# Kernel tuning notes

Measured on AMD Instinct MI355X. Metric: run time of the kernel, lower is better.

The kernel has to match this reference:

```python
import jax, jax.numpy as jnp
import numpy as np

N = 65536          # nodes
E = 1_048_576      # edges (avg degree 16)
IN_DIM = 16        # input_irreps = 16x0e
OUT_DIM = 8        # output_irreps = 8x0e
S_MUL = 32         # hidden 0e multiplicity
V_MUL = 16         # hidden 1o multiplicity
HID = S_MUL + 3 * V_MUL  # 80
LAYERS = 3
DEG = 16.0


def fctp(feat, eattr, w1, w2, w3, w4):
    """FullyConnectedTensorProduct(hidden x '1x0e+1x1o' -> hidden) per edge.
    Paths: 0e*0e->0e, 1o*1o->0e (dot, CG 1/sqrt(3)), 0e*1o->1o, 1o*0e->1o.
    Path weights mix multiplicities; e3nn-style fan-in normalization."""
    s1 = feat[:, :S_MUL]                         # [E, 32]
    v1 = feat[:, S_MUL:].reshape(-1, V_MUL, 3)   # [E, 16, 3]
    s2 = eattr[:, 0]                             # [E]
    v2 = eattr[:, 1:4]                           # [E, 3]
    c = 1.0 / np.sqrt(2.0)  # two paths per output irrep
    out_s = c * (jnp.einsum('ea,e,ac->ec', s1, s2, w1) / np.sqrt(S_MUL)
                 + jnp.einsum('eak,ek,ac->ec', v1, v2, w2) / np.sqrt(3.0 * V_MUL))
    out_v = c * (jnp.einsum('ea,ek,ac->eck', s1, v2, w3) / np.sqrt(S_MUL)
                 + jnp.einsum('eak,e,ac->eck', v1, s2, w4) / np.sqrt(V_MUL))
    return jnp.concatenate([out_s, out_v.reshape(-1, 3 * V_MUL)], axis=-1)


def setup_inputs() -> dict:
    key = jax.random.key(0)
    ks = jax.random.split(key, 12)
    inp = {
        'x': jax.random.normal(ks[0], (N, IN_DIM), jnp.float32),
        'edge_index': jax.random.randint(ks[1], (2, E), 0, N, jnp.int64 if jax.config.jax_enable_x64 else jnp.int32),
        'edge_attr': jax.random.normal(ks[2], (E, 4), jnp.float32),
        'W_in': jax.random.normal(ks[3], (IN_DIM, HID), jnp.float32) / np.sqrt(IN_DIM),
        'b_in': jnp.zeros((HID,), jnp.float32),
        'tp_w1': jax.random.normal(ks[4], (LAYERS, S_MUL, S_MUL), jnp.float32),
        'tp_w2': jax.random.normal(ks[5], (LAYERS, V_MUL, S_MUL), jnp.float32),
        'tp_w3': jax.random.normal(ks[6], (LAYERS, S_MUL, V_MUL), jnp.float32),
        'tp_w4': jax.random.normal(ks[7], (LAYERS, V_MUL, V_MUL), jnp.float32),
        'W_out': jax.random.normal(ks[8], (HID, OUT_DIM), jnp.float32) / np.sqrt(HID),
        'b_out': jnp.zeros((OUT_DIM,), jnp.float32),
    }
    return inp


def reference(x, edge_index, edge_attr, W_in, b_in, tp_w1, tp_w2, tp_w3, tp_w4, W_out, b_out):
    src, dst = edge_index[0], edge_index[1]
    h = x @ W_in + b_in                                   # [N, 80]
    for l in range(LAYERS):
        m = fctp(h[src], edge_attr, tp_w1[l], tp_w2[l], tp_w3[l], tp_w4[l])  # [E, 80]
        h = jax.ops.segment_sum(m, dst, num_segments=N) / np.sqrt(DEG)       # [N, 80]
    h = jax.nn.relu(h)
    return h @ W_out + b_out                              # [N, 8]
```

## Files before the change

kernel.cpp:

```cpp
#include <hip/hip_runtime.h>

#define NN 65536
#define NE 1048576
#define HID 80

typedef unsigned int u32;
typedef unsigned short u16;
typedef unsigned long long u64;

__device__ __forceinline__ u16 f2bf(float f) {
  u32 u = __float_as_uint(f);
  u = (u + 0x7fffu + ((u >> 16) & 1u)) >> 16;
  return (u16)u;
}
__device__ __forceinline__ float bfhi(u32 packed) {
  return __uint_as_float(packed & 0xffff0000u);
}
__device__ __forceinline__ float bflo(u32 packed) {
  return __uint_as_float(packed << 16);
}

__global__ __launch_bounds__(256) void k_in(const float* __restrict__ x,
    const float* __restrict__ W, const float* __restrict__ b,
    u16* __restrict__ hmain, u16* __restrict__ htail) {
  int idx = blockIdx.x * 256 + threadIdx.x;
  if (idx >= NN * HID) return;
  int n = idx / HID, l = idx % HID;
  const float* xr = x + n * 16;
  float acc = b[l];
#pragma unroll
  for (int k = 0; k < 16; k++) acc += xr[k] * W[k * HID + l];
  u16 v = f2bf(acc);
  if (l < 64) hmain[(size_t)n * 64 + l] = v;
  else htail[(size_t)n * 16 + (l - 64)] = v;
}

__global__ __launch_bounds__(256) void k_hist(const int* __restrict__ dst,
    int* __restrict__ counts, int* __restrict__ rank, int* __restrict__ dcnt) {
  if (blockIdx.x == 0 && threadIdx.x < 16) dcnt[threadIdx.x] = 0;
  int base = blockIdx.x * 2048 + threadIdx.x;
#pragma unroll
  for (int k = 0; k < 8; k++) {
    int idx = base + k * 256;
    rank[idx] = atomicAdd(&counts[dst[idx]], 1);
  }
}

__global__ __launch_bounds__(256) void k_nb_scan(const int* __restrict__ counts,
    int* __restrict__ offsets, int* __restrict__ blocksum,
    int* __restrict__ dcnt, int* __restrict__ brank, int* __restrict__ bidx) {
  __shared__ int sc[256];
  int t = threadIdx.x;
  if (blockIdx.x < 64) {
    int base = blockIdx.x * 1024 + t * 4;
    int p0 = (counts[base] + 7) & ~7;
    int p1 = (counts[base + 1] + 7) & ~7;
    int p2 = (counts[base + 2] + 7) & ~7;
    int p3 = (counts[base + 3] + 7) & ~7;
    int s = p0 + p1 + p2 + p3;
    sc[t] = s;
    __syncthreads();
    for (int d = 1; d < 256; d <<= 1) {
      int v = (t >= d) ? sc[t - d] : 0;
      __syncthreads();
      sc[t] += v;
      __syncthreads();
    }
    int excl = sc[t] - s;
    offsets[base] = excl;
    offsets[base + 1] = excl + p0;
    offsets[base + 2] = excl + p0 + p1;
    offsets[base + 3] = excl + p0 + p1 + p2;
    if (t == 255) blocksum[blockIdx.x] = sc[255];
  } else {
    int n = (blockIdx.x - 64) * 256 + t;
    int degp = (counts[n] + 7) & ~7;
    int b = 15 - min(degp >> 3, 15);
    int lane = t & 63;
    int base = 0;
#pragma unroll 1
    for (int bb = 0; bb < 16; bb++) {
      u64 m = __ballot(b == bb);
      if (b == bb) {
        int leader = __ffsll((long long)m) - 1;
        int lr = __popcll(m & ((lane == 63) ? ~0ull >> 1 : ((1ull << lane) - 1)));
        int bs = 0;
        if (lane == leader) bs = atomicAdd(&dcnt[bb], __popcll(m));
        bs = __shfl(bs, leader, 64);
        base = bs + lr;
      }
    }
    brank[n] = base;
    bidx[n] = b;
  }
}

__global__ __launch_bounds__(64) void k_scan2(int* __restrict__ blocksum,
                                              int* __restrict__ dcnt) {
  int t = threadIdx.x;
  if (blockIdx.x == 0) {
    int v = blocksum[t];
    int incl = v;
#pragma unroll
    for (int d = 1; d < 64; d <<= 1) {
      int o = __shfl_up(incl, d, 64);
      if (t >= d) incl += o;
    }
    blocksum[t] = incl - v;
  } else {
    if (t >= 16) return;
    int v = dcnt[t];
    int incl = v;
#pragma unroll
    for (int d = 1; d < 16; d <<= 1) {
      int o = __shfl_up(incl, d, 64);
      if (t >= d) incl += o;
    }
    dcnt[t] = incl - v;
  }
}

__global__ __launch_bounds__(256) void k_node_fin(int* __restrict__ offsets,
    const int* __restrict__ blocksum, const int* __restrict__ counts,
    u16* __restrict__ esrc, uint2* __restrict__ eat,
    const int* __restrict__ dcnt, const int* __restrict__ brank,
    const int* __restrict__ bidx, int* __restrict__ nperm) {
  int n = blockIdx.x * 256 + threadIdx.x;
  int off = offsets[n] + blocksum[n >> 10];
  offsets[n] = off;
  int deg = counts[n];
  int degp = (deg + 7) & ~7;
  uint2 z2 = make_uint2(0u, 0u);
  for (int e = deg; e < degp; e++) {
    esrc[off + e] = 0;
    eat[off + e] = z2;
  }
  nperm[dcnt[bidx[n]] + brank[n]] = n;
}

__global__ __launch_bounds__(256) void k_fill(const int* __restrict__ src,
    const int* __restrict__ dst, const float4* __restrict__ eattr,
    const int* __restrict__ offsets, const int* __restrict__ rank,
    u16* __restrict__ esrc, uint2* __restrict__ eat) {
  int base = blockIdx.x * 2048 + threadIdx.x;
#pragma unroll
  for (int k = 0; k < 8; k++) {
    int idx = base + k * 256;
    int d = dst[idx];
    float4 ea = eattr[idx];
    int s = src[idx];
    u32 c01 = (u32)f2bf(ea.x) | ((u32)f2bf(ea.y) << 16);
    u32 c23 = (u32)f2bf(ea.z) | ((u32)f2bf(ea.w) << 16);
    int pos = offsets[d] + rank[idx];
    esrc[pos] = (u16)s;
    eat[pos] = make_uint2(c01, c23);
  }
}

template <int LAST>
__global__ __launch_bounds__(128, 3) void k_msg(const u16* __restrict__ hmain,
    const u16* __restrict__ htail, u16* __restrict__ omain,
    u16* __restrict__ otail,
    const float* __restrict__ w1, const float* __restrict__ w2,
    const float* __restrict__ w3, const float* __restrict__ w4,
    const int* __restrict__ offsets, const int* __restrict__ counts,
    const int* __restrict__ nperm, const u16* __restrict__ esrc,
    const uint2* __restrict__ eat, const float* __restrict__ Wout,
    const float* __restrict__ bout, float* __restrict__ outp) {
  __shared__ float Rlds[8][4][81];
  int tid = threadIdx.x;
  const int q = tid >> 4;
  const int c = tid & 15;
  const int n = nperm[blockIdx.x * 8 + q];

  float R[4][5];
#pragma unroll
  for (int j = 0; j < 4; j++)
#pragma unroll
    for (int i = 0; i < 5; i++) R[j][i] = 0.f;

  const int start = offsets[n];
  const int degp = (counts[n] + 7) & ~7;
  const int B = degp >> 3;
  const uint2* hrow = (const uint2*)hmain + c;
  const u16* trow = htail + c;

  int i = 0;
  for (; i + 2 <= B; i += 2) {
    const int baseA = start + 8 * i;
    const int baseB = baseA + 8;
    u32 sA[8], sB[8];
    uint2 aA[8], aB[8];
#pragma unroll
    for (int k = 0; k < 8; k++) sA[k] = esrc[baseA + k];
#pragma unroll
    for (int k = 0; k < 8; k++) aA[k] = eat[baseA + k];
#pragma unroll
    for (int k = 0; k < 8; k++) sB[k] = esrc[baseB + k];
#pragma unroll
    for (int k = 0; k < 8; k++) aB[k] = eat[baseB + k];
    uint2 hA[8], hB[8];
    u32 tA[8], tB[8];
#pragma unroll
    for (int k = 0; k < 8; k++) {
      size_t s16 = (size_t)sA[k] * 16;
      hA[k] = hrow[s16];
      tA[k] = trow[s16];
    }
#pragma unroll
    for (int k = 0; k < 8; k++) {
      size_t s16 = (size_t)sB[k] * 16;
      hB[k] = hrow[s16];
      tB[k] = trow[s16];
    }
#pragma unroll
    for (int k = 0; k < 8; k++) {
      float A0 = bflo(hA[k].x), A1 = bfhi(hA[k].x);
      float A2 = bflo(hA[k].y), A3 = bfhi(hA[k].y);
      float A4 = bflo(tA[k]);
      float f0 = bflo(aA[k].x), f1 = bfhi(aA[k].x);
      float f2 = bflo(aA[k].y), f3 = bfhi(aA[k].y);
      R[0][0] += f0 * A0; R[0][1] += f0 * A1; R[0][2] += f0 * A2;
      R[0][3] += f0 * A3; R[0][4] += f0 * A4;
      R[1][0] += f1 * A0; R[1][1] += f1 * A1; R[1][2] += f1 * A2;
      R[1][3] += f1 * A3; R[1][4] += f1 * A4;
      R[2][0] += f2 * A0; R[2][1] += f2 * A1; R[2][2] += f2 * A2;
      R[2][3] += f2 * A3; R[2][4] += f2 * A4;
      R[3][0] += f3 * A0; R[3][1] += f3 * A1; R[3][2] += f3 * A2;
      R[3][3] += f3 * A3; R[3][4] += f3 * A4;
    }
#pragma unroll
    for (int k = 0; k < 8; k++) {
      float A0 = bflo(hB[k].x), A1 = bfhi(hB[k].x);
      float A2 = bflo(hB[k].y), A3 = bfhi(hB[k].y);
      float A4 = bflo(tB[k]);
      float f0 = bflo(aB[k].x), f1 = bfhi(aB[k].x);
      float f2 = bflo(aB[k].y), f3 = bfhi(aB[k].y);
      R[0][0] += f0 * A0; R[0][1] += f0 * A1; R[0][2] += f0 * A2;
      R[0][3] += f0 * A3; R[0][4] += f0 * A4;
      R[1][0] += f1 * A0; R[1][1] += f1 * A1; R[1][2] += f1 * A2;
      R[1][3] += f1 * A3; R[1][4] += f1 * A4;
      R[2][0] += f2 * A0; R[2][1] += f2 * A1; R[2][2] += f2 * A2;
      R[2][3] += f2 * A3; R[2][4] += f2 * A4;
      R[3][0] += f3 * A0; R[3][1] += f3 * A1; R[3][2] += f3 * A2;
      R[3][3] += f3 * A3; R[3][4] += f3 * A4;
    }
  }
  if (i < B) {
    const int baseA = start + 8 * i;
    u32 sA[8];
    uint2 aA[8];
#pragma unroll
    for (int k = 0; k < 8; k++) sA[k] = esrc[baseA + k];
#pragma unroll
    for (int k = 0; k < 8; k++) aA[k] = eat[baseA + k];
    uint2 hA[8];
    u32 tA[8];
#pragma unroll
    for (int k = 0; k < 8; k++) {
      size_t s16 = (size_t)sA[k] * 16;
      hA[k] = hrow[s16];
      tA[k] = trow[s16];
    }
#pragma unroll
    for (int k = 0; k < 8; k++) {
      float A0 = bflo(hA[k].x), A1 = bfhi(hA[k].x);
      float A2 = bflo(hA[k].y), A3 = bfhi(hA[k].y);
      float A4 = bflo(tA[k]);
      float f0 = bflo(aA[k].x), f1 = bfhi(aA[k].x);
      float f2 = bflo(aA[k].y), f3 = bfhi(aA[k].y);
      R[0][0] += f0 * A0; R[0][1] += f0 * A1; R[0][2] += f0 * A2;
      R[0][3] += f0 * A3; R[0][4] += f0 * A4;
      R[1][0] += f1 * A0; R[1][1] += f1 * A1; R[1][2] += f1 * A2;
      R[1][3] += f1 * A3; R[1][4] += f1 * A4;
      R[2][0] += f2 * A0; R[2][1] += f2 * A1; R[2][2] += f2 * A2;
      R[2][3] += f2 * A3; R[2][4] += f2 * A4;
      R[3][0] += f3 * A0; R[3][1] += f3 * A1; R[3][2] += f3 * A2;
      R[3][3] += f3 * A3; R[3][4] += f3 * A4;
    }
  }

#pragma unroll
  for (int j = 0; j < 4; j++) {
#pragma unroll
    for (int k = 0; k < 4; k++) Rlds[q][j][4 * c + k] = R[j][k];
    Rlds[q][j][64 + c] = R[j][4];
  }

  const float C1 = 0.03125f;
  const float C2 = 0.025515518f;
  const float C3 = 0.03125f;
  const float C4 = 0.044194174f;

  u16* opm = omain + (size_t)n * 64;

  float s0 = 0.f, s1 = 0.f;
#pragma unroll
  for (int a = 0; a < 32; a++) {
    float rs = Rlds[q][0][a];
    s0 += rs * w1[a * 32 + c];
    s1 += rs * w1[a * 32 + c + 16];
  }
  float t0 = 0.f, t1 = 0.f;
#pragma unroll
  for (int a = 0; a < 16; a++) {
    float T = Rlds[q][1][32 + 3 * a] + Rlds[q][2][33 + 3 * a] +
              Rlds[q][3][34 + 3 * a];
    t0 += T * w2[a * 32 + c];
    t1 += T * w2[a * 32 + c + 16];
  }

  float y[8];
  if (LAST) {
#pragma unroll
    for (int j = 0; j < 8; j++) y[j] = 0.f;
    float vs0 = C1 * s0 + C2 * t0;
    float vs1 = C1 * s1 + C2 * t1;
    vs0 = vs0 > 0.f ? vs0 : 0.f;
    vs1 = vs1 > 0.f ? vs1 : 0.f;
#pragma unroll
    for (int j = 0; j < 8; j++)
      y[j] += vs0 * Wout[c * 8 + j] + vs1 * Wout[(c + 16) * 8 + j];
  } else {
    opm[c] = f2bf(C1 * s0 + C2 * t0);
    opm[c + 16] = f2bf(C1 * s1 + C2 * t1);
  }

#pragma unroll
  for (int v2 = 0; v2 < 3; v2++) {
    int c2 = 32 + 16 * v2 + c;
    int cv = (c2 - 32) / 3, k = (c2 - 32) % 3;
    float a3 = 0.f, a4 = 0.f;
#pragma unroll
    for (int a = 0; a < 32; a++) a3 += Rlds[q][k + 1][a] * w3[a * 16 + cv];
#pragma unroll
    for (int a = 0; a < 16; a++)
      a4 += Rlds[q][0][32 + 3 * a + k] * w4[a * 16 + cv];
    float val = C3 * a3 + C4 * a4;
    if (LAST) {
      val = val > 0.f ? val : 0.f;
#pragma unroll
      for (int j = 0; j < 8; j++) y[j] += val * Wout[c2 * 8 + j];
    } else {
      u16 v = f2bf(val);
      if (v2 < 2) opm[32 + 16 * v2 + c] = v;
      else otail[(size_t)n * 16 + c] = v;
    }
  }

  if (LAST) {
#pragma unroll
    for (int m = 1; m <= 8; m <<= 1) {
#pragma unroll
      for (int j = 0; j < 8; j++) y[j] += __shfl_xor(y[j], m, 64);
    }
    float w = y[0];
#pragma unroll
    for (int j = 1; j < 8; j++)
      if (c == j) w = y[j];
    if (c < 8) outp[(size_t)n * 8 + c] = w + bout[c];
  }
}

extern "C" void kernel_launch(void* const* d_in, const int* in_sizes, int n_in,
                              void* d_out, int out_size, void* d_ws,
                              size_t ws_size, hipStream_t stream) {
  const float* x = (const float*)d_in[0];
  const int* ei = (const int*)d_in[1];
  const float* eattr = (const float*)d_in[2];
  const float* W_in = (const float*)d_in[3];
  const float* b_in = (const float*)d_in[4];
  const float* tp_w1 = (const float*)d_in[5];
  const float* tp_w2 = (const float*)d_in[6];
  const float* tp_w3 = (const float*)d_in[7];
  const float* tp_w4 = (const float*)d_in[8];
  const float* W_out = (const float*)d_in[9];
  const float* b_out = (const float*)d_in[10];
  float* out = (float*)d_out;

  char* ws = (char*)d_ws;
  size_t off = 0;
  auto alloc = [&](size_t bytes) {
    void* p = ws + off;
    off += (bytes + 255) & ~size_t(255);
    return p;
  };
  const size_t NEP = (size_t)NE + 8 * (size_t)NN;
  u16* hm_a = (u16*)alloc((size_t)NN * 64 * 2);
  u16* ht_a = (u16*)alloc((size_t)NN * 16 * 2);
  u16* hm_b = (u16*)alloc((size_t)NN * 64 * 2);
  u16* ht_b = (u16*)alloc((size_t)NN * 16 * 2);
  int* counts = (int*)alloc((size_t)NN * 4);
  int* offsets = (int*)alloc((size_t)NN * 4);
  int* blocksum = (int*)alloc(64 * 4);
  int* rank = (int*)alloc((size_t)NE * 4);
  int* dcnt = (int*)alloc(16 * 4);
  int* brank = (int*)alloc((size_t)NN * 4);
  int* bidx = (int*)alloc((size_t)NN * 4);
  int* nperm = (int*)alloc((size_t)NN * 4);
  u16* esrc = (u16*)alloc(NEP * 2);
  uint2* eat = (uint2*)alloc(NEP * 8);

  const int* src = ei;
  const int* dst = ei + NE;

  hipMemsetAsync(counts, 0, (size_t)NN * 4, stream);
  k_in<<<(NN * HID + 255) / 256, 256, 0, stream>>>(x, W_in, b_in, hm_a, ht_a);
  k_hist<<<NE / 2048, 256, 0, stream>>>(dst, counts, rank, dcnt);
  k_nb_scan<<<64 + NN / 256, 256, 0, stream>>>(counts, offsets, blocksum, dcnt,
                                               brank, bidx);
  k_scan2<<<2, 64, 0, stream>>>(blocksum, dcnt);
  k_node_fin<<<NN / 256, 256, 0, stream>>>(offsets, blocksum, counts, esrc,
                                           eat, dcnt, brank, bidx, nperm);
  k_fill<<<NE / 2048, 256, 0, stream>>>(src, dst, (const float4*)eattr,
                                        offsets, rank, esrc, eat);

  u16* hmi = hm_a;
  u16* hti = ht_a;
  u16* hmo = hm_b;
  u16* hto = ht_b;
  for (int l = 0; l < 2; l++) {
    k_msg<0><<<NN / 8, 128, 0, stream>>>(hmi, hti, hmo, hto, tp_w1 + l * 1024,
                                         tp_w2 + l * 512, tp_w3 + l * 512,
                                         tp_w4 + l * 256, offsets, counts,
                                         nperm, esrc, eat, W_out, b_out, out);
    u16* t;
    t = hmi; hmi = hmo; hmo = t;
    t = hti; hti = hto; hto = t;
  }
  k_msg<1><<<NN / 8, 128, 0, stream>>>(hmi, hti, hmo, hto, tp_w1 + 2048,
                                       tp_w2 + 1024, tp_w3 + 1024, tp_w4 + 512,
                                       offsets, counts, nperm, esrc, eat,
                                       W_out, b_out, out);
}
```

Baseline: 393.1 us.

## Pack edge src and attrs into 16-byte records, vectorize input projection

Merges the separate esrc (u16) and eat (uint2) edge arrays into a single padded 16-byte record per edge, loaded with one nontemporal 128-bit load in the message kernel. The input projection kernel now computes 8 outputs per thread with vectorized stores and also zeroes the counts array, which removes a memset. k_fill uses nontemporal loads for the streaming inputs. The cost is that edge storage grows from 10 to 16 bytes per edge, which raises edge traffic in each of the three message passes, in exchange for fewer, wider load instructions.

```diff
diff --git a/kernel.cpp b/kernel.cpp
--- a/kernel.cpp
+++ b/kernel.cpp
@@ -7,6 +7,10 @@
 typedef unsigned int u32;
 typedef unsigned short u16;
 typedef unsigned long long u64;
+
+typedef unsigned int v4u __attribute__((ext_vector_type(4)));
+typedef float v4f __attribute__((ext_vector_type(4)));
+typedef int v4i __attribute__((ext_vector_type(4)));
 
 __device__ __forceinline__ u16 f2bf(float f) {
   u32 u = __float_as_uint(f);
@@ -19,20 +23,47 @@
 __device__ __forceinline__ float bflo(u32 packed) {
   return __uint_as_float(packed << 16);
 }
+__device__ __forceinline__ uint4 ntload4(const uint4* p) {
+  v4u v = __builtin_nontemporal_load((const v4u*)p);
+  return make_uint4(v.x, v.y, v.z, v.w);
+}
+__device__ __forceinline__ float4 ntload4f(const float4* p) {
+  v4f v = __builtin_nontemporal_load((const v4f*)p);
+  return make_float4(v.x, v.y, v.z, v.w);
+}
+__device__ __forceinline__ int ntloadi(const int* p) {
+  return __builtin_nontemporal_load(p);
+}
 
 __global__ __launch_bounds__(256) void k_in(const float* __restrict__ x,
     const float* __restrict__ W, const float* __restrict__ b,
-    u16* __restrict__ hmain, u16* __restrict__ htail) {
+    u16* __restrict__ hmain, u16* __restrict__ htail,
+    int* __restrict__ counts) {
   int idx = blockIdx.x * 256 + threadIdx.x;
-  if (idx >= NN * HID) return;
-  int n = idx / HID, l = idx % HID;
-  const float* xr = x + n * 16;
-  float acc = b[l];
-#pragma unroll
-  for (int k = 0; k < 16; k++) acc += xr[k] * W[k * HID + l];
-  u16 v = f2bf(acc);
-  if (l < 64) hmain[(size_t)n * 64 + l] = v;
-  else htail[(size_t)n * 16 + (l - 64)] = v;
+  if (idx < NN) counts[idx] = 0;
+  if (idx >= NN * 10) return;
+  int n = idx / 10, part = idx % 10;
+  const float4* xr = (const float4*)(x + (size_t)n * 16);
+  float4 x0 = xr[0], x1 = xr[1], x2 = xr[2], x3 = xr[3];
+  const float xs[16] = {x0.x, x0.y, x0.z, x0.w, x1.x, x1.y, x1.z, x1.w,
+                        x2.x, x2.y, x2.z, x2.w, x3.x, x3.y, x3.z, x3.w};
+  float acc[8];
+#pragma unroll
+  for (int j = 0; j < 8; j++) acc[j] = b[part * 8 + j];
+#pragma unroll
+  for (int k = 0; k < 16; k++) {
+#pragma unroll
+    for (int j = 0; j < 8; j++) acc[j] += xs[k] * W[k * HID + part * 8 + j];
+  }
+  u32 p0 = (u32)f2bf(acc[0]) | ((u32)f2bf(acc[1]) << 16);
+  u32 p1 = (u32)f2bf(acc[2]) | ((u32)f2bf(acc[3]) << 16);
+  u32 p2 = (u32)f2bf(acc[4]) | ((u32)f2bf(acc[5]) << 16);
+  u32 p3 = (u32)f2bf(acc[6]) | ((u32)f2bf(acc[7]) << 16);
+  uint4 vv = make_uint4(p0, p1, p2, p3);
+  if (part < 8)
+    *(uint4*)(hmain + (size_t)n * 64 + part * 8) = vv;
+  else
+    *(uint4*)(htail + (size_t)n * 16 + (part - 8) * 8) = vv;
 }
 
 __global__ __launch_bounds__(256) void k_hist(const int* __restrict__ dst,
@@ -122,38 +153,34 @@
 
 __global__ __launch_bounds__(256) void k_node_fin(int* __restrict__ offsets,
     const int* __restrict__ blocksum, const int* __restrict__ counts,
-    u16* __restrict__ esrc, uint2* __restrict__ eat,
-    const int* __restrict__ dcnt, const int* __restrict__ brank,
-    const int* __restrict__ bidx, int* __restrict__ nperm) {
+    uint4* __restrict__ erec, const int* __restrict__ dcnt,
+    const int* __restrict__ brank, const int* __restrict__ bidx,
+    int* __restrict__ nperm) {
   int n = blockIdx.x * 256 + threadIdx.x;
   int off = offsets[n] + blocksum[n >> 10];
   offsets[n] = off;
   int deg = counts[n];
   int degp = (deg + 7) & ~7;
-  uint2 z2 = make_uint2(0u, 0u);
-  for (int e = deg; e < degp; e++) {
-    esrc[off + e] = 0;
-    eat[off + e] = z2;
-  }
+  uint4 z = make_uint4(0u, 0u, 0u, 0u);
+  for (int e = deg; e < degp; e++) erec[off + e] = z;
   nperm[dcnt[bidx[n]] + brank[n]] = n;
 }
 
 __global__ __launch_bounds__(256) void k_fill(const int* __restrict__ src,
     const int* __restrict__ dst, const float4* __restrict__ eattr,
     const int* __restrict__ offsets, const int* __restrict__ rank,
-    u16* __restrict__ esrc, uint2* __restrict__ eat) {
+    uint4* __restrict__ erec) {
   int base = blockIdx.x * 2048 + threadIdx.x;
 #pragma unroll
   for (int k = 0; k < 8; k++) {
     int idx = base + k * 256;
-    int d = dst[idx];
-    float4 ea = eattr[idx];
-    int s = src[idx];
+    int d = ntloadi(dst + idx);
+    float4 ea = ntload4f(eattr + idx);
+    int s = ntloadi(src + idx);
     u32 c01 = (u32)f2bf(ea.x) | ((u32)f2bf(ea.y) << 16);
     u32 c23 = (u32)f2bf(ea.z) | ((u32)f2bf(ea.w) << 16);
     int pos = offsets[d] + rank[idx];
-    esrc[pos] = (u16)s;
-    eat[pos] = make_uint2(c01, c23);
+    erec[pos] = make_uint4((u32)s, c01, c23, 0u);
   }
 }
 
@@ -164,9 +191,9 @@
     const float* __restrict__ w1, const float* __restrict__ w2,
     const float* __restrict__ w3, const float* __restrict__ w4,
     const int* __restrict__ offsets, const int* __restrict__ counts,
-    const int* __restrict__ nperm, const u16* __restrict__ esrc,
-    const uint2* __restrict__ eat, const float* __restrict__ Wout,
-    const float* __restrict__ bout, float* __restrict__ outp) {
+    const int* __restrict__ nperm, const uint4* __restrict__ erec,
+    const float* __restrict__ Wout, const float* __restrict__ bout,
+    float* __restrict__ outp) {
   __shared__ float Rlds[8][4][81];
   int tid = threadIdx.x;
   const int q = tid >> 4;
@@ -189,27 +216,22 @@
   for (; i + 2 <= B; i += 2) {
     const int baseA = start + 8 * i;
     const int baseB = baseA + 8;
-    u32 sA[8], sB[8];
-    uint2 aA[8], aB[8];
-#pragma unroll
-    for (int k = 0; k < 8; k++) sA[k] = esrc[baseA + k];
-#pragma unroll
-    for (int k = 0; k < 8; k++) aA[k] = eat[baseA + k];
-#pragma unroll
-    for (int k = 0; k < 8; k++) sB[k] = esrc[baseB + k];
-#pragma unroll
-    for (int k = 0; k < 8; k++) aB[k] = eat[baseB + k];
+    uint4 rA[8], rB[8];
+#pragma unroll
+    for (int k = 0; k < 8; k++) rA[k] = ntload4(&erec[baseA + k]);
+#pragma unroll
+    for (int k = 0; k < 8; k++) rB[k] = ntload4(&erec[baseB + k]);
     uint2 hA[8], hB[8];
     u32 tA[8], tB[8];
 #pragma unroll
     for (int k = 0; k < 8; k++) {
-      size_t s16 = (size_t)sA[k] * 16;
+      size_t s16 = (size_t)rA[k].x * 16;
       hA[k] = hrow[s16];
       tA[k] = trow[s16];
     }
 #pragma unroll
     for (int k = 0; k < 8; k++) {
-      size_t s16 = (size_t)sB[k] * 16;
+      size_t s16 = (size_t)rB[k].x * 16;
       hB[k] = hrow[s16];
       tB[k] = trow[s16];
     }
@@ -218,8 +240,8 @@
       float A0 = bflo(hA[k].x), A1 = bfhi(hA[k].x);
       float A2 = bflo(hA[k].y), A3 = bfhi(hA[k].y);
       float A4 = bflo(tA[k]);
-      float f0 = bflo(aA[k].x), f1 = bfhi(aA[k].x);
-      float f2 = bflo(aA[k].y), f3 = bfhi(aA[k].y);
+      float f0 = bflo(rA[k].y), f1 = bfhi(rA[k].y);
+      float f2 = bflo(rA[k].z), f3 = bfhi(rA[k].z);
       R[0][0] += f0 * A0; R[0][1] += f0 * A1; R[0][2] += f0 * A2;
       R[0][3] += f0 * A3; R[0][4] += f0 * A4;
       R[1][0] += f1 * A0; R[1][1] += f1 * A1; R[1][2] += f1 * A2;
@@ -234,8 +256,8 @@
       float A0 = bflo(hB[k].x), A1 = bfhi(hB[k].x);
       float A2 = bflo(hB[k].y), A3 = bfhi(hB[k].y);
       float A4 = bflo(tB[k]);
-      float f0 = bflo(aB[k].x), f1 = bfhi(aB[k].x);
-      float f2 = bflo(aB[k].y), f3 = bfhi(aB[k].y);
+      float f0 = bflo(rB[k].y), f1 = bfhi(rB[k].y);
+      float f2 = bflo(rB[k].z), f3 = bfhi(rB[k].z);
       R[0][0] += f0 * A0; R[0][1] += f0 * A1; R[0][2] += f0 * A2;
       R[0][3] += f0 * A3; R[0][4] += f0 * A4;
       R[1][0] += f1 * A0; R[1][1] += f1 * A1; R[1][2] += f1 * A2;
@@ -248,17 +270,14 @@
   }
   if (i < B) {
     const int baseA = start + 8 * i;
-    u32 sA[8];
-    uint2 aA[8];
-#pragma unroll
-    for (int k = 0; k < 8; k++) sA[k] = esrc[baseA + k];
-#pragma unroll
-    for (int k = 0; k < 8; k++) aA[k] = eat[baseA + k];
+    uint4 rA[8];
+#pragma unroll
+    for (int k = 0; k < 8; k++) rA[k] = ntload4(&erec[baseA + k]);
     uint2 hA[8];
     u32 tA[8];
 #pragma unroll
     for (int k = 0; k < 8; k++) {
-      size_t s16 = (size_t)sA[k] * 16;
+      size_t s16 = (size_t)rA[k].x * 16;
       hA[k] = hrow[s16];
       tA[k] = trow[s16];
     }
@@ -267,8 +286,8 @@
       float A0 = bflo(hA[k].x), A1 = bfhi(hA[k].x);
       float A2 = bflo(hA[k].y), A3 = bfhi(hA[k].y);
       float A4 = bflo(tA[k]);
-      float f0 = bflo(aA[k].x), f1 = bfhi(aA[k].x);
-      float f2 = bflo(aA[k].y), f3 = bfhi(aA[k].y);
+      float f0 = bflo(rA[k].y), f1 = bfhi(rA[k].y);
+      float f2 = bflo(rA[k].z), f3 = bfhi(rA[k].z);
       R[0][0] += f0 * A0; R[0][1] += f0 * A1; R[0][2] += f0 * A2;
       R[0][3] += f0 * A3; R[0][4] += f0 * A4;
       R[1][0] += f1 * A0; R[1][1] += f1 * A1; R[1][2] += f1 * A2;
@@ -398,22 +417,21 @@
   int* brank = (int*)alloc((size_t)NN * 4);
   int* bidx = (int*)alloc((size_t)NN * 4);
   int* nperm = (int*)alloc((size_t)NN * 4);
-  u16* esrc = (u16*)alloc(NEP * 2);
-  uint2* eat = (uint2*)alloc(NEP * 8);
+  uint4* erec = (uint4*)alloc(NEP * 16);
 
   const int* src = ei;
   const int* dst = ei + NE;
 
-  hipMemsetAsync(counts, 0, (size_t)NN * 4, stream);
-  k_in<<<(NN * HID + 255) / 256, 256, 0, stream>>>(x, W_in, b_in, hm_a, ht_a);
+  k_in<<<(NN * 10 + 255) / 256, 256, 0, stream>>>(x, W_in, b_in, hm_a, ht_a,
+                                                  counts);
   k_hist<<<NE / 2048, 256, 0, stream>>>(dst, counts, rank, dcnt);
   k_nb_scan<<<64 + NN / 256, 256, 0, stream>>>(counts, offsets, blocksum, dcnt,
                                                brank, bidx);
   k_scan2<<<2, 64, 0, stream>>>(blocksum, dcnt);
-  k_node_fin<<<NN / 256, 256, 0, stream>>>(offsets, blocksum, counts, esrc,
-                                           eat, dcnt, brank, bidx, nperm);
+  k_node_fin<<<NN / 256, 256, 0, stream>>>(offsets, blocksum, counts, erec,
+                                           dcnt, brank, bidx, nperm);
   k_fill<<<NE / 2048, 256, 0, stream>>>(src, dst, (const float4*)eattr,
-                                        offsets, rank, esrc, eat);
+                                        offsets, rank, erec);
 
   u16* hmi = hm_a;
   u16* hti = ht_a;
@@ -423,13 +441,13 @@
     k_msg<0><<<NN / 8, 128, 0, stream>>>(hmi, hti, hmo, hto, tp_w1 + l * 1024,
                                          tp_w2 + l * 512, tp_w3 + l * 512,
                                          tp_w4 + l * 256, offsets, counts,
-                                         nperm, esrc, eat, W_out, b_out, out);
+                                         nperm, erec, W_out, b_out, out);
     u16* t;
     t = hmi; hmi = hmo; hmo = t;
     t = hti; hti = hto; hto = t;
   }
   k_msg<1><<<NN / 8, 128, 0, stream>>>(hmi, hti, hmo, hto, tp_w1 + 2048,
                                        tp_w2 + 1024, tp_w3 + 1024, tp_w4 + 512,
-                                       offsets, counts, nperm, esrc, eat,
+                                       offsets, counts, nperm, erec,
                                        W_out, b_out, out);
 }
```

Result: slower. 404.6 us (+2.9%).
